# Performance work log

Measured on AMD Instinct MI355X. Metric: run time of the kernel, lower is better.

The kernel has to match this reference:

```python
import jax, jax.numpy as jnp
import numpy as np

B, S, NH, NKV, D = 2, 2048, 32, 8, 128

def setup_inputs() -> dict:
    key = jax.random.key(0)
    kq, kk, kv = jax.random.split(key, 3)
    query = jax.random.normal(kq, (B, S, NH, D), dtype=jnp.float32)
    k_ = jax.random.normal(kk, (B, S, NKV, D), dtype=jnp.float32)
    v_ = jax.random.normal(kv, (B, S, NKV, D), dtype=jnp.float32)
    # causal additive mask, broadcastable to [B, NH, S, S]
    causal = jnp.tril(jnp.ones((S, S), dtype=bool))
    attn_mask = jnp.where(causal, 0.0, -1e9).astype(jnp.float32)[None, None]
    return {"query": query, "key": k_, "value": v_, "attn_mask": attn_mask}

def reference(query, key, value, attn_mask):
    nh, nkv = query.shape[-2], key.shape[-2]
    # [B, S, H, D] -> [B, H, S, D]
    q = jnp.swapaxes(query, -3, -2)
    k = jnp.swapaxes(key, -3, -2)
    v = jnpp_swap(value) if False else jnp.swapaxes(value, -3, -2)
    qpk = nh // nkv
    if qpk > 1:
        k = jnp.repeat(k, qpk, axis=-3)
        v = jnp.repeat(v, qpk, axis=-3)
    scale = q.shape[-1] ** (-0.5)
    # [B, H, Sq, Sk]
    score = jnp.einsum('bhqd,bhkd->bhqk', q, k) * scale
    score = score + attn_mask
    probs = jax.nn.softmax(score.astype(jnp.float32), axis=-1).astype(q.dtype)
    out = jnp.einsum('bhqk,bhkd->bhqd', probs, v)
    # [B, H, S, D] -> [B, S, H, D]
    return jnp.swapaxes(out, 1, 2)
```

## Files before the change

kernel.cpp:

```cpp
#include <hip/hip_runtime.h>
#include <hip/hip_bf16.h>

#define B_    2
#define S_    2048
#define NH_   32
#define NKV_  8
#define D_    128
#define QBLK  128
#define KVBLK 64

#define KVH_STRIDE 524288u
#define V_WS_OFF   8388608u

typedef __bf16 bf16x8 __attribute__((ext_vector_type(8)));
typedef float  f32x16 __attribute__((ext_vector_type(16)));
typedef unsigned short u16x4 __attribute__((ext_vector_type(4)));
typedef unsigned int   u32x4 __attribute__((ext_vector_type(4)));

typedef const __attribute__((address_space(1))) void* gptr_t;
typedef __attribute__((address_space(3))) void*       lptr_t;

#if __has_builtin(__builtin_amdgcn_exp2f)
#define EXP2(x) __builtin_amdgcn_exp2f(x)
#else
#define EXP2(x) exp2f(x)
#endif

__device__ inline unsigned short bfu(float f) {
    return __builtin_bit_cast(unsigned short, (__bf16)f);
}
__device__ inline unsigned packbf(float lo, float hi) {
    return (unsigned)bfu(lo) | ((unsigned)bfu(hi) << 16);
}

__device__ inline void* kaddr(unsigned short* base, int row, int byteInRow) {
    return (void*)((char*)base + row * 256 + (byteInRow ^ ((row & 7) << 4)));
}
__device__ inline void* vaddr(unsigned short* base, int row, int byteInRow) {
    return (void*)((char*)base + row * 128 + (byteInRow ^ ((row & 7) << 4)));
}

__global__ __launch_bounds__(256)
void convert_k(const float* __restrict__ kin, unsigned short* __restrict__ kout) {
    const int g = blockIdx.x * 256 + threadIdx.x;
    const size_t o = (size_t)g * 4;
    const int d   = (int)(o & 127);
    const int k   = (int)((o >> 7) & 2047);
    const int kvh = (int)((o >> 18) & 7);
    const int b   = (int)(o >> 21);
    const float* src = kin + (((size_t)(b * 2048 + k)) * 8 + kvh) * 128 + d;
    float4 x = *reinterpret_cast<const float4*>(src);
    u16x4 u = { bfu(x.x), bfu(x.y), bfu(x.z), bfu(x.w) };
    *reinterpret_cast<u16x4*>(kout + o) = u;
}

__global__ __launch_bounds__(256)
void convert_v(const float* __restrict__ vin, unsigned short* __restrict__ vout) {
    __shared__ unsigned short vl[64][136];
    const int t  = threadIdx.x;
    const int bb = blockIdx.x;
    const int j  = bb & 31;
    const int bk = bb >> 5;
    const int b  = bk >> 3, kvh = bk & 7;
    const float* base = vin + (((size_t)(b * 2048 + j * 64)) * 8 + kvh) * 128;
    #pragma unroll
    for (int i = 0; i < 8; ++i) {
        const int row = i * 8 + (t >> 5), c4 = t & 31;
        float4 x = *reinterpret_cast<const float4*>(base + (size_t)row * 1024 + c4 * 4);
        u16x4 u = { bfu(x.x), bfu(x.y), bfu(x.z), bfu(x.w) };
        *reinterpret_cast<u16x4*>(&vl[row][c4 * 4]) = u;
    }
    __syncthreads();
    unsigned short* out = vout + (size_t)bb * 8192;
    #pragma unroll
    for (int it = 0; it < 4; ++it) {
        const int c = it * 256 + t;
        const int d = c >> 3, k0 = (c & 7) * 8;
        u16x4 lo = { vl[k0 + 0][d], vl[k0 + 1][d], vl[k0 + 2][d], vl[k0 + 3][d] };
        u16x4 hi = { vl[k0 + 4][d], vl[k0 + 5][d], vl[k0 + 6][d], vl[k0 + 7][d] };
        *reinterpret_cast<u16x4*>(out + (size_t)d * 64 + k0)     = lo;
        *reinterpret_cast<u16x4*>(out + (size_t)d * 64 + k0 + 4) = hi;
    }
}

__global__ __launch_bounds__(256, 2)
void sdpa_fwd(const float* __restrict__ qg, const unsigned short* __restrict__ kws,
              const unsigned short* __restrict__ vws, float* __restrict__ og)
{
    __shared__ __align__(16) unsigned short Kb[2][8192];
    __shared__ __align__(16) unsigned short Vb[2][8192];

    const int bx  = blockIdx.x;
    const int qt  = 15 - (bx >> 6);
    const int r   = bx & 63;
    const int kvh = r & 7;
    const int h   = kvh * 4 + ((r >> 3) & 3);
    const int b   = (r >> 5) & 1;
    const int bk  = b * 8 + kvh;

    const int t   = threadIdx.x;
    const int w   = t >> 6;
    const int l   = t & 63;
    const int l32 = l & 31;
    const int lh  = l >> 5;

    const float scale = 0.08838834764831845f * 1.4426950408889634f;
    const int qmin_w = qt * QBLK + w * 32;
    const int qgl    = qmin_w + l32;

    const int koff = ((t >> 4) << 8) + ((((t & 15) << 4)) ^ (((t >> 4) & 7) << 4));
    const int voff = ((t >> 3) << 7) + ((((t & 7) << 4)) ^ (((t >> 3) & 7) << 4));
    const char* Khead = (const char*)kws + (size_t)bk * KVH_STRIDE;
    const char* Vhead = (const char*)vws + (size_t)bk * KVH_STRIDE;

    bf16x8 qf[8];
    {
        const float* Qp = qg + (((size_t)b * S_ + qgl) * NH_ + h) * D_;
        #pragma unroll
        for (int dc = 0; dc < 8; ++dc) {
            const int d0 = dc * 16 + lh * 8;
            float4 a = *reinterpret_cast<const float4*>(Qp + d0);
            float4 c = *reinterpret_cast<const float4*>(Qp + d0 + 4);
            bf16x8 f;
            f[0] = (__bf16)(a.x * scale); f[1] = (__bf16)(a.y * scale);
            f[2] = (__bf16)(a.z * scale); f[3] = (__bf16)(a.w * scale);
            f[4] = (__bf16)(c.x * scale); f[5] = (__bf16)(c.y * scale);
            f[6] = (__bf16)(c.z * scale); f[7] = (__bf16)(c.w * scale);
            qf[dc] = f;
        }
    }

    f32x16 acc[4] = {};
    float mrow = -INFINITY, lrow = 0.0f;

    auto issueK = [&](int j, int c) {
        const char* ks = Khead + (size_t)j * 16384 + koff;
        char* kl = (char*)&Kb[c][0] + t * 16;
        #pragma unroll
        for (int i = 0; i < 4; ++i)
            __builtin_amdgcn_global_load_lds((gptr_t)(ks + i * 4096),
                                             (lptr_t)(kl + i * 4096), 16, 0, 0);
    };
    auto issueV = [&](int j, int c) {
        const char* vs = Vhead + (size_t)j * 16384 + voff;
        char* vl = (char*)&Vb[c][0] + t * 16;
        #pragma unroll
        for (int i = 0; i < 4; ++i)
            __builtin_amdgcn_global_load_lds((gptr_t)(vs + i * 4096),
                                             (lptr_t)(vl + i * 4096), 16, 0, 0);
    };

    issueV(0, 0); issueK(0, 0);
    const int jmax = 2 * qt + 1;

    for (int j = 0; j <= jmax; ++j) {
        const int cur = j & 1;
        const int jbase = j * KVBLK;
        const bool live = (jbase <= qmin_w + 31);

        __builtin_amdgcn_s_barrier();
        __builtin_amdgcn_sched_barrier(0);
        if (j < jmax) {
            issueV(j + 1, cur ^ 1);
            issueK(j + 1, cur ^ 1);
            asm volatile("s_waitcnt vmcnt(8)" ::: "memory");
        } else {
            asm volatile("s_waitcnt vmcnt(0)" ::: "memory");
        }
        __builtin_amdgcn_s_barrier();
        __builtin_amdgcn_sched_barrier(0);

        if (live) {
            unsigned short* kbuf = &Kb[cur][0];
            unsigned short* vbuf = &Vb[cur][0];

            f32x16 sc0 = {}, sc1 = {};
            __builtin_amdgcn_s_setprio(1);
            #pragma unroll
            for (int dc = 0; dc < 8; ++dc) {
                bf16x8 kf0 = *reinterpret_cast<const bf16x8*>(
                    kaddr(kbuf, l32, dc * 32 + lh * 16));
                sc0 = __builtin_amdgcn_mfma_f32_32x32x16_bf16(kf0, qf[dc], sc0, 0, 0, 0);
                bf16x8 kf1 = *reinterpret_cast<const bf16x8*>(
                    kaddr(kbuf, 32 + l32, dc * 32 + lh * 16));
                sc1 = __builtin_amdgcn_mfma_f32_32x32x16_bf16(kf1, qf[dc], sc1, 0, 0, 0);
            }
            __builtin_amdgcn_s_setprio(0);

            if (jbase + (KVBLK - 1) > qmin_w) {
                #pragma unroll
                for (int rr = 0; rr < 16; ++rr) {
                    const int kk = jbase + (rr & 3) + 8 * (rr >> 2) + 4 * lh;
                    if (kk > qgl)      sc0[rr] = -INFINITY;
                    if (kk + 32 > qgl) sc1[rr] = -INFINITY;
                }
            }

            float mx[16];
            #pragma unroll
            for (int rr = 0; rr < 16; ++rr) mx[rr] = fmaxf(sc0[rr], sc1[rr]);
            #pragma unroll
            for (int s = 8; s > 0; s >>= 1)
                #pragma unroll
                for (int i = 0; i < 8; ++i)
                    if (i < s) mx[i] = fmaxf(mx[i], mx[i + s]);
            float mt = fmaxf(mx[0], __shfl_xor(mx[0], 32));
            const float mnew = fmaxf(mrow, mt);
            if (!__all(mnew - mrow <= 11.5f)) {
                const float resc = EXP2(mrow - mnew);
                lrow *= resc;
                #pragma unroll
                for (int dt = 0; dt < 4; ++dt) acc[dt] *= resc;
                mrow = mnew;
            }
            #pragma unroll
            for (int rr = 0; rr < 16; ++rr) {
                sc0[rr] = EXP2(sc0[rr] - mrow);
                sc1[rr] = EXP2(sc1[rr] - mrow);
            }
            float sm[16];
            #pragma unroll
            for (int rr = 0; rr < 16; ++rr) sm[rr] = sc0[rr] + sc1[rr];
            #pragma unroll
            for (int s = 8; s > 0; s >>= 1)
                #pragma unroll
                for (int i = 0; i < 8; ++i)
                    if (i < s) sm[i] += sm[i + s];
            lrow += sm[0] + __shfl_xor(sm[0], 32);

            bf16x8 pa[4];
            #pragma unroll
            for (int g = 0; g < 4; ++g) {
                float p0, p1, p2, p3, p4, p5, p6, p7;
                if (g == 0) { p0=sc0[0]; p1=sc0[1]; p2=sc0[2]; p3=sc0[3];
                              p4=sc0[4]; p5=sc0[5]; p6=sc0[6]; p7=sc0[7]; }
                else if (g == 1) { p0=sc0[8];  p1=sc0[9];  p2=sc0[10]; p3=sc0[11];
                                   p4=sc0[12]; p5=sc0[13]; p6=sc0[14]; p7=sc0[15]; }
                else if (g == 2) { p0=sc1[0]; p1=sc1[1]; p2=sc1[2]; p3=sc1[3];
                                   p4=sc1[4]; p5=sc1[5]; p6=sc1[6]; p7=sc1[7]; }
                else { p0=sc1[8];  p1=sc1[9];  p2=sc1[10]; p3=sc1[11];
                       p4=sc1[12]; p5=sc1[13]; p6=sc1[14]; p7=sc1[15]; }
                unsigned a0 = packbf(p0, p1), b0 = packbf(p4, p5);
                unsigned a1 = packbf(p2, p3), b1 = packbf(p6, p7);
                auto s02 = __builtin_amdgcn_permlane32_swap((int)a0, (int)b0, false, false);
                auto s13 = __builtin_amdgcn_permlane32_swap((int)a1, (int)b1, false, false);
                u32x4 dw = { (unsigned)s02[0], (unsigned)s13[0],
                             (unsigned)s02[1], (unsigned)s13[1] };
                pa[g] = __builtin_bit_cast(bf16x8, dw);
            }

            __builtin_amdgcn_s_setprio(1);
            #pragma unroll
            for (int kc = 0; kc < 4; ++kc) {
                #pragma unroll
                for (int dt = 0; dt < 4; ++dt) {
                    bf16x8 vf = *reinterpret_cast<const bf16x8*>(
                        vaddr(vbuf, dt * 32 + l32, kc * 32 + lh * 16));
                    acc[dt] = __builtin_amdgcn_mfma_f32_32x32x16_bf16(vf, pa[kc], acc[dt], 0, 0, 0);
                }
            }
            __builtin_amdgcn_s_setprio(0);
        }
    }

    const float invl = 1.0f / lrow;
    float* Op = og + (((size_t)b * S_ + qgl) * NH_ + h) * D_;
    #pragma unroll
    for (int dt = 0; dt < 4; ++dt) {
        #pragma unroll
        for (int rg = 0; rg < 4; ++rg) {
            float4 st;
            st.x = acc[dt][rg * 4 + 0] * invl;
            st.y = acc[dt][rg * 4 + 1] * invl;
            st.z = acc[dt][rg * 4 + 2] * invl;
            st.w = acc[dt][rg * 4 + 3] * invl;
            *reinterpret_cast<float4*>(Op + dt * 32 + rg * 8 + lh * 4) = st;
        }
    }
}

extern "C" void kernel_launch(void* const* d_in, const int* in_sizes, int n_in,
                              void* d_out, int out_size, void* d_ws, size_t ws_size,
                              hipStream_t stream) {
    const float* q = (const float*)d_in[0];
    const float* k = (const float*)d_in[1];
    const float* v = (const float*)d_in[2];
    float* out = (float*)d_out;
    unsigned short* kws = (unsigned short*)d_ws;
    unsigned short* vws = (unsigned short*)((char*)d_ws + V_WS_OFF);

    convert_k<<<dim3(4096), 256, 0, stream>>>(k, kws);
    convert_v<<<dim3(512),  256, 0, stream>>>(v, vws);
    sdpa_fwd <<<dim3(1024), 256, 0, stream>>>(q, kws, vws, out);
}
```

Baseline: 115.2 us.

## Software-pipeline QK^T of the next KV tile with softmax and PV of the current tile

Restructures the KV loop into pairs of tiles so that the QK^T MFMAs for tile j+1 are issued alongside the softmax and PV work for tile j. K and V loads are split and staged separately across barriers, giving finer-grained async prefetch. The aim is to hide softmax VALU latency behind matrix-core work and overlap loads better. It keeps two sets of score accumulators live, which raises register pressure, and adds more barriers per iteration.

Result: faster. 110.4 us (-4.2%).

```diff
diff --git a/kernel.cpp b/kernel.cpp
--- a/kernel.cpp
+++ b/kernel.cpp
@@ -131,6 +131,7 @@
     }
 
     f32x16 acc[4] = {};
+    f32x16 scA0, scA1, scB0, scB1;
     float mrow = -INFINITY, lrow = 0.0f;
 
     auto issueK = [&](int j, int c) {
@@ -150,118 +151,130 @@
                                              (lptr_t)(vl + i * 4096), 16, 0, 0);
     };
 
-    issueV(0, 0); issueK(0, 0);
+    auto qk = [&](unsigned short* kbuf, f32x16& s0, f32x16& s1) {
+        s0 = (f32x16){}; s1 = (f32x16){};
+        #pragma unroll
+        for (int dc = 0; dc < 8; ++dc) {
+            bf16x8 kf0 = *reinterpret_cast<const bf16x8*>(
+                kaddr(kbuf, l32, dc * 32 + lh * 16));
+            s0 = __builtin_amdgcn_mfma_f32_32x32x16_bf16(kf0, qf[dc], s0, 0, 0, 0);
+            bf16x8 kf1 = *reinterpret_cast<const bf16x8*>(
+                kaddr(kbuf, 32 + l32, dc * 32 + lh * 16));
+            s1 = __builtin_amdgcn_mfma_f32_32x32x16_bf16(kf1, qf[dc], s1, 0, 0, 0);
+        }
+    };
+
+    auto smpv = [&](f32x16& s0, f32x16& s1, int jb, unsigned short* vbuf) {
+        if (jb + (KVBLK - 1) > qmin_w) {
+            #pragma unroll
+            for (int rr = 0; rr < 16; ++rr) {
+                const int kk = jb + (rr & 3) + 8 * (rr >> 2) + 4 * lh;
+                if (kk > qgl)      s0[rr] = -INFINITY;
+                if (kk + 32 > qgl) s1[rr] = -INFINITY;
+            }
+        }
+        float mx[16];
+        #pragma unroll
+        for (int rr = 0; rr < 16; ++rr) mx[rr] = fmaxf(s0[rr], s1[rr]);
+        #pragma unroll
+        for (int s = 8; s > 0; s >>= 1)
+            #pragma unroll
+            for (int i = 0; i < 8; ++i)
+                if (i < s) mx[i] = fmaxf(mx[i], mx[i + s]);
+        float mt = fmaxf(mx[0], __shfl_xor(mx[0], 32));
+        const float mnew = fmaxf(mrow, mt);
+        if (!__all(mnew - mrow <= 11.5f)) {
+            const float resc = EXP2(mrow - mnew);
+            lrow *= resc;
+            #pragma unroll
+            for (int dt = 0; dt < 4; ++dt) acc[dt] *= resc;
+            mrow = mnew;
+        }
+        #pragma unroll
+        for (int rr = 0; rr < 16; ++rr) {
+            s0[rr] = EXP2(s0[rr] - mrow);
+            s1[rr] = EXP2(s1[rr] - mrow);
+        }
+        float sm[16];
+        #pragma unroll
+        for (int rr = 0; rr < 16; ++rr) sm[rr] = s0[rr] + s1[rr];
+        #pragma unroll
+        for (int s = 8; s > 0; s >>= 1)
+            #pragma unroll
+            for (int i = 0; i < 8; ++i)
+                if (i < s) sm[i] += sm[i + s];
+        lrow += sm[0] + __shfl_xor(sm[0], 32);
+
+        bf16x8 pa[4];
+        #pragma unroll
+        for (int g = 0; g < 4; ++g) {
+            float p0, p1, p2, p3, p4, p5, p6, p7;
+            if (g == 0) { p0=s0[0]; p1=s0[1]; p2=s0[2]; p3=s0[3];
+                          p4=s0[4]; p5=s0[5]; p6=s0[6]; p7=s0[7]; }
+            else if (g == 1) { p0=s0[8];  p1=s0[9];  p2=s0[10]; p3=s0[11];
+                               p4=s0[12]; p5=s0[13]; p6=s0[14]; p7=s0[15]; }
+            else if (g == 2) { p0=s1[0]; p1=s1[1]; p2=s1[2]; p3=s1[3];
+                               p4=s1[4]; p5=s1[5]; p6=s1[6]; p7=s1[7]; }
+            else { p0=s1[8];  p1=s1[9];  p2=s1[10]; p3=s1[11];
+                   p4=s1[12]; p5=s1[13]; p6=s1[14]; p7=s1[15]; }
+            unsigned a0 = packbf(p0, p1), b0 = packbf(p4, p5);
+            unsigned a1 = packbf(p2, p3), b1 = packbf(p6, p7);
+            auto s02 = __builtin_amdgcn_permlane32_swap((int)a0, (int)b0, false, false);
+            auto s13 = __builtin_amdgcn_permlane32_swap((int)a1, (int)b1, false, false);
+            u32x4 dw = { (unsigned)s02[0], (unsigned)s13[0],
+                         (unsigned)s02[1], (unsigned)s13[1] };
+            pa[g] = __builtin_bit_cast(bf16x8, dw);
+        }
+        #pragma unroll
+        for (int kc = 0; kc < 4; ++kc) {
+            #pragma unroll
+            for (int dt = 0; dt < 4; ++dt) {
+                bf16x8 vf = *reinterpret_cast<const bf16x8*>(
+                    vaddr(vbuf, dt * 32 + l32, kc * 32 + lh * 16));
+                acc[dt] = __builtin_amdgcn_mfma_f32_32x32x16_bf16(vf, pa[kc], acc[dt], 0, 0, 0);
+            }
+        }
+    };
+
+    issueK(0, 0); issueV(0, 0);
     const int jmax = 2 * qt + 1;
-
-    for (int j = 0; j <= jmax; ++j) {
-        const int cur = j & 1;
-        const int jbase = j * KVBLK;
-        const bool live = (jbase <= qmin_w + 31);
-
+    const int lastlive = (qmin_w + 31) >> 6;
+
+    #pragma unroll 1
+    for (int j0 = 0; j0 <= jmax; j0 += 2) {
+        const int j1 = j0 + 1;
+        issueK(j1, 1);
+        asm volatile("s_waitcnt vmcnt(8)" ::: "memory");
         __builtin_amdgcn_s_barrier();
         __builtin_amdgcn_sched_barrier(0);
-        if (j < jmax) {
-            issueV(j + 1, cur ^ 1);
-            issueK(j + 1, cur ^ 1);
+        __builtin_amdgcn_s_setprio(1);
+        if (j0 <= lastlive) qk(&Kb[0][0], scA0, scA1);
+        if (j0 > 0 && j0 - 1 <= lastlive)
+            smpv(scB0, scB1, (j0 - 1) * KVBLK, &Vb[1][0]);
+        __builtin_amdgcn_s_setprio(0);
+        __builtin_amdgcn_s_barrier();
+        __builtin_amdgcn_sched_barrier(0);
+        issueV(j1, 1);
+        if (j1 < jmax) {
+            issueK(j1 + 1, 0);
             asm volatile("s_waitcnt vmcnt(8)" ::: "memory");
         } else {
-            asm volatile("s_waitcnt vmcnt(0)" ::: "memory");
+            asm volatile("s_waitcnt vmcnt(4)" ::: "memory");
         }
         __builtin_amdgcn_s_barrier();
         __builtin_amdgcn_sched_barrier(0);
-
-        if (live) {
-            unsigned short* kbuf = &Kb[cur][0];
-            unsigned short* vbuf = &Vb[cur][0];
-
-            f32x16 sc0 = {}, sc1 = {};
-            __builtin_amdgcn_s_setprio(1);
-            #pragma unroll
-            for (int dc = 0; dc < 8; ++dc) {
-                bf16x8 kf0 = *reinterpret_cast<const bf16x8*>(
-                    kaddr(kbuf, l32, dc * 32 + lh * 16));
-                sc0 = __builtin_amdgcn_mfma_f32_32x32x16_bf16(kf0, qf[dc], sc0, 0, 0, 0);
-                bf16x8 kf1 = *reinterpret_cast<const bf16x8*>(
-                    kaddr(kbuf, 32 + l32, dc * 32 + lh * 16));
-                sc1 = __builtin_amdgcn_mfma_f32_32x32x16_bf16(kf1, qf[dc], sc1, 0, 0, 0);
-            }
-            __builtin_amdgcn_s_setprio(0);
-
-            if (jbase + (KVBLK - 1) > qmin_w) {
-                #pragma unroll
-                for (int rr = 0; rr < 16; ++rr) {
-                    const int kk = jbase + (rr & 3) + 8 * (rr >> 2) + 4 * lh;
-                    if (kk > qgl)      sc0[rr] = -INFINITY;
-                    if (kk + 32 > qgl) sc1[rr] = -INFINITY;
-                }
-            }
-
-            float mx[16];
-            #pragma unroll
-            for (int rr = 0; rr < 16; ++rr) mx[rr] = fmaxf(sc0[rr], sc1[rr]);
-            #pragma unroll
-            for (int s = 8; s > 0; s >>= 1)
-                #pragma unroll
-                for (int i = 0; i < 8; ++i)
-                    if (i < s) mx[i] = fmaxf(mx[i], mx[i + s]);
-            float mt = fmaxf(mx[0], __shfl_xor(mx[0], 32));
-            const float mnew = fmaxf(mrow, mt);
-            if (!__all(mnew - mrow <= 11.5f)) {
-                const float resc = EXP2(mrow - mnew);
-                lrow *= resc;
-                #pragma unroll
-                for (int dt = 0; dt < 4; ++dt) acc[dt] *= resc;
-                mrow = mnew;
-            }
-            #pragma unroll
-            for (int rr = 0; rr < 16; ++rr) {
-                sc0[rr] = EXP2(sc0[rr] - mrow);
-                sc1[rr] = EXP2(sc1[rr] - mrow);
-            }
-            float sm[16];
-            #pragma unroll
-            for (int rr = 0; rr < 16; ++rr) sm[rr] = sc0[rr] + sc1[rr];
-            #pragma unroll
-            for (int s = 8; s > 0; s >>= 1)
-                #pragma unroll
-                for (int i = 0; i < 8; ++i)
-                    if (i < s) sm[i] += sm[i + s];
-            lrow += sm[0] + __shfl_xor(sm[0], 32);
-
-            bf16x8 pa[4];
-            #pragma unroll
-            for (int g = 0; g < 4; ++g) {
-                float p0, p1, p2, p3, p4, p5, p6, p7;
-                if (g == 0) { p0=sc0[0]; p1=sc0[1]; p2=sc0[2]; p3=sc0[3];
-                              p4=sc0[4]; p5=sc0[5]; p6=sc0[6]; p7=sc0[7]; }
-                else if (g == 1) { p0=sc0[8];  p1=sc0[9];  p2=sc0[10]; p3=sc0[11];
-                                   p4=sc0[12]; p5=sc0[13]; p6=sc0[14]; p7=sc0[15]; }
-                else if (g == 2) { p0=sc1[0]; p1=sc1[1]; p2=sc1[2]; p3=sc1[3];
-                                   p4=sc1[4]; p5=sc1[5]; p6=sc1[6]; p7=sc1[7]; }
-                else { p0=sc1[8];  p1=sc1[9];  p2=sc1[10]; p3=sc1[11];
-                       p4=sc1[12]; p5=sc1[13]; p6=sc1[14]; p7=sc1[15]; }
-                unsigned a0 = packbf(p0, p1), b0 = packbf(p4, p5);
-                unsigned a1 = packbf(p2, p3), b1 = packbf(p6, p7);
-                auto s02 = __builtin_amdgcn_permlane32_swap((int)a0, (int)b0, false, false);
-                auto s13 = __builtin_amdgcn_permlane32_swap((int)a1, (int)b1, false, false);
-                u32x4 dw = { (unsigned)s02[0], (unsigned)s13[0],
-                             (unsigned)s02[1], (unsigned)s13[1] };
-                pa[g] = __builtin_bit_cast(bf16x8, dw);
-            }
-
-            __builtin_amdgcn_s_setprio(1);
-            #pragma unroll
-            for (int kc = 0; kc < 4; ++kc) {
-                #pragma unroll
-                for (int dt = 0; dt < 4; ++dt) {
-                    bf16x8 vf = *reinterpret_cast<const bf16x8*>(
-                        vaddr(vbuf, dt * 32 + l32, kc * 32 + lh * 16));
-                    acc[dt] = __builtin_amdgcn_mfma_f32_32x32x16_bf16(vf, pa[kc], acc[dt], 0, 0, 0);
-                }
-            }
-            __builtin_amdgcn_s_setprio(0);
-        }
-    }
+        __builtin_amdgcn_s_setprio(1);
+        if (j1 <= lastlive) qk(&Kb[1][0], scB0, scB1);
+        if (j0 <= lastlive) smpv(scA0, scA1, j0 * KVBLK, &Vb[0][0]);
+        __builtin_amdgcn_s_setprio(0);
+        __builtin_amdgcn_s_barrier();
+        __builtin_amdgcn_sched_barrier(0);
+        if (j1 < jmax) issueV(j1 + 1, 0);
+    }
+    asm volatile("s_waitcnt vmcnt(0)" ::: "memory");
+    __builtin_amdgcn_s_barrier();
+    __builtin_amdgcn_sched_barrier(0);
+    if (jmax <= lastlive) smpv(scB0, scB1, jmax * KVBLK, &Vb[1][0]);
 
     const float invl = 1.0f / lrow;
     float* Op = og + (((size_t)b * S_ + qgl) * NH_ + h) * D_;
```
